# Optimization experiments

Hardware: AMD Instinct MI355X
Metric: run time of the kernel (lower is better)

The kernel has to match this reference:

```python
import jax, jax.numpy as jnp
import numpy as np


def _ln(x, g, b, eps=1e-6):
    m = jnp.mean(x, axis=-1, keepdims=True)
    v = jnp.var(x, axis=-1, keepdims=True)
    return (x - m) * jax.lax.rsqrt(v + eps) * g + b


def setup_inputs():
    key = jax.random.key(0)
    ks = jax.random.split(key, 16)
    B, Hs, Ws, D = 2, 48, 48, 768
    heads, P = 6, 4
    L = Hs * Ws                # feat tokens (single level, 1/16 scale)
    N = 21 * (Hs * Ws // 4)    # query tokens: 16n + 4n + n multi-scale layout
    hidden = int(D * 0.25)
    s = 0.02
    return {
        "query": jax.random.normal(ks[0], (B, N, D), jnp.float32),
        "reference_points": jax.random.uniform(ks[1], (B, N, 1, 2), jnp.float32),
        "feat": jax.random.normal(ks[2], (B, L, D), jnp.float32),
        "spatial_shapes": jnp.array([[Hs, Ws]], jnp.int32),
        "level_start_index": jnp.array([0], jnp.int32),
        "H": Hs, "W": Ws,
        "qn_g": jnp.ones((D,), jnp.float32), "qn_b": jnp.zeros((D,), jnp.float32),
        "fn_g": jnp.ones((D,), jnp.float32), "fn_b": jnp.zeros((D,), jnp.float32),
        "Wv": jax.random.normal(ks[3], (D, D), jnp.float32) * s, "bv": jnp.zeros((D,), jnp.float32),
        "Woff": jax.random.normal(ks[4], (D, heads * P * 2), jnp.float32) * s,
        "boff": jax.random.normal(ks[5], (heads * P * 2,), jnp.float32) * s,
        "Wattn": jax.random.normal(ks[6], (D, heads * P), jnp.float32) * s,
        "battn": jnp.zeros((heads * P,), jnp.float32),
        "Wo": jax.random.normal(ks[7], (D, D), jnp.float32) * s, "bo": jnp.zeros((D,), jnp.float32),
        "ffn_g": jnp.ones((D,), jnp.float32), "ffn_b": jnp.zeros((D,), jnp.float32),
        "W1": jax.random.normal(ks[8], (D, hidden), jnp.float32) * s, "b1": jnp.zeros((hidden,), jnp.float32),
        "dw_w": jax.random.normal(ks[9], (hidden, 1, 3, 3), jnp.float32) * s, "dw_b": jnp.zeros((hidden,), jnp.float32),
        "W2": jax.random.normal(ks[10], (hidden, D), jnp.float32) * s, "b2": jnp.zeros((D,), jnp.float32),
    }


def reference(query, reference_points, feat, spatial_shapes, level_start_index, H, W,
              qn_g, qn_b, fn_g, fn_b, Wv, bv, Woff, boff, Wattn, battn, Wo, bo,
              ffn_g, ffn_b, W1, b1, dw_w, dw_b, W2, b2):
    B, N, D = query.shape
    heads, P = 6, 4
    dh = D // heads
    hidden = W1.shape[1]
    # ---- MSDeformAttn (single level) ----
    qn = _ln(query, qn_g, qn_b)
    fn = _ln(feat, fn_g, fn_b)
    value = (fn @ Wv + bv).reshape(B, -1, heads, dh)           # (B,L,h,dh)
    off = (qn @ Woff + boff).reshape(B, N, heads, 1, P, 2)
    aw = jax.nn.softmax((qn @ Wattn + battn).reshape(B, N, heads, P), axis=-1)
    # offset normalizer = [W_l, H_l]
    norm = jnp.stack([spatial_shapes[..., 1], spatial_shapes[..., 0]], -1).astype(qn.dtype)
    loc = reference_points[:, :, None, :, None, :] + off / norm[None, None, None, :, None, :]
    loc = loc[:, :, :, 0]  # (B,N,heads,P,2) single level
    # grid_sample bilinear, align_corners=False, zero padding
    x = loc[..., 0] * W - 0.5
    y = loc[..., 1] * H - 0.5
    x0 = jnp.floor(x); y0 = jnp.floor(y)
    wx = x - x0; wy = y - y0
    x0 = x0.astype(jnp.int32); y0 = y0.astype(jnp.int32)
    value_t = value.transpose(0, 2, 1, 3)  # (B,heads,L,dh)

    def corner(xi, yi, w):
        valid = (xi >= 0) & (xi < W) & (yi >= 0) & (yi < H)
        idx = jnp.clip(yi, 0, H - 1) * W + jnp.clip(xi, 0, W - 1)
        idx = idx.transpose(0, 2, 1, 3).reshape(B, heads, N * P)
        v = jnp.take_along_axis(value_t, idx[..., None], axis=2)  # (B,h,N*P,dh)
        wm = jnp.where(valid, w, 0.0).transpose(0, 2, 1, 3).reshape(B, heads, N * P)
        return v * wm[..., None]

    sampled = (corner(x0, y0, (1 - wx) * (1 - wy)) + corner(x0 + 1, y0, wx * (1 - wy))
               + corner(x0, y0 + 1, (1 - wx) * wy) + corner(x0 + 1, y0 + 1, wx * wy))
    sampled = sampled.reshape(B, heads, N, P, dh)
    attn = jnp.einsum('bhnpd,bnhp->bnhd', sampled, aw).reshape(B, N, D) @ Wo + bo
    query = query + attn
    # ---- ConvFFN (hidden=dim*cffn_ratio, multi-scale DWConv) ----
    h = _ln(query, ffn_g, ffn_b) @ W1 + b1
    n = N // 21

    def dw(t, hh, ww):
        img = t.transpose(0, 2, 1).reshape(B, hidden, hh, ww)
        out = jax.lax.conv_general_dilated(img, dw_w, (1, 1), 'SAME', feature_group_count=hidden)
        return (out + dw_b[None, :, None, None]).reshape(B, hidden, hh * ww).transpose(0, 2, 1)

    h = jnp.concatenate([dw(h[:, :16 * n], 2 * H, 2 * W),
                         dw(h[:, 16 * n:20 * n], H, W),
                         dw(h[:, 20 * n:], H // 2, W // 2)], axis=1)
    h = jax.nn.gelu(h, approximate=False)
    return query + (h @ W2 + b2)
```

## Files before the change

kernel.cpp:

```cpp
#include <hip/hip_runtime.h>
#include <math.h>

#define BB 2
#define NN 12096
#define LL 2304
#define DD 768
#define HID 192
#define HS 48
#define WS 48

typedef unsigned short u16;
typedef unsigned int u32;
typedef __attribute__((ext_vector_type(8))) __bf16 bf16x8;
typedef __attribute__((ext_vector_type(8))) unsigned short u16x8;
typedef __attribute__((ext_vector_type(4))) float f32x4;

__device__ __forceinline__ u16 f2bf(float f) {
  u32 x = __builtin_bit_cast(u32, f);
  u32 r = (x + 0x7fffu + ((x >> 16) & 1u)) >> 16;
  return (u16)r;
}
__device__ __forceinline__ float bf2f(u16 u) {
  u32 x = ((u32)u) << 16;
  return __builtin_bit_cast(float, x);
}

template <typename T>
__device__ __forceinline__ void ln_row4(const T* xr, const float* g, const float* bta, u16* yr, int t) {
  float v0, v1, v2, v3;
  if constexpr (sizeof(T) == 2) {
    ushort4 u = *(const ushort4*)(xr + 4 * t);
    v0 = bf2f(u.x); v1 = bf2f(u.y); v2 = bf2f(u.z); v3 = bf2f(u.w);
  } else {
    float4 f = *(const float4*)(xr + 4 * t);
    v0 = f.x; v1 = f.y; v2 = f.z; v3 = f.w;
  }
  float s = v0 + v1 + v2 + v3;
  float s2 = v0 * v0 + v1 * v1 + v2 * v2 + v3 * v3;
#pragma unroll
  for (int off = 32; off; off >>= 1) {
    s += __shfl_down(s, off, 64);
    s2 += __shfl_down(s2, off, 64);
  }
  __shared__ float red[6];
  __shared__ float mv[2];
  int wave = t >> 6, lane = t & 63;
  if (lane == 0) { red[wave] = s; red[3 + wave] = s2; }
  __syncthreads();
  if (t == 0) {
    float ts = red[0] + red[1] + red[2];
    float ts2 = red[3] + red[4] + red[5];
    float m = ts * (1.f / DD);
    float var = ts2 * (1.f / DD) - m * m;
    mv[0] = m;
    mv[1] = rsqrtf(var + 1e-6f);
  }
  __syncthreads();
  float m = mv[0], rs = mv[1];
  float4 gv = *(const float4*)(g + 4 * t);
  float4 bv = *(const float4*)(bta + 4 * t);
  ushort4 o;
  o.x = f2bf((v0 - m) * rs * gv.x + bv.x);
  o.y = f2bf((v1 - m) * rs * gv.y + bv.y);
  o.z = f2bf((v2 - m) * rs * gv.z + bv.z);
  o.w = f2bf((v3 - m) * rs * gv.w + bv.w);
  *(ushort4*)(yr + 4 * t) = o;
}

template <typename T>
__global__ __launch_bounds__(192) void ln_kernel(const T* __restrict__ x,
                                                 const float* __restrict__ g,
                                                 const float* __restrict__ bta,
                                                 u16* __restrict__ y) {
  size_t row = blockIdx.x;
  ln_row4<T>(x + row * DD, g, bta, y + row * DD, threadIdx.x);
}

__global__ __launch_bounds__(192) void ln_dual_kernel(const float* __restrict__ xq,
                                                      const float* __restrict__ gq,
                                                      const float* __restrict__ bq,
                                                      u16* __restrict__ yq,
                                                      const float* __restrict__ xf,
                                                      const float* __restrict__ gf,
                                                      const float* __restrict__ bf_,
                                                      u16* __restrict__ yf,
                                                      int Mq) {
  size_t row = blockIdx.x;
  if (row < (size_t)Mq)
    ln_row4<float>(xq + row * DD, gq, bq, yq + row * DD, threadIdx.x);
  else {
    size_t r = row - Mq;
    ln_row4<float>(xf + r * DD, gf, bf_, yf + r * DD, threadIdx.x);
  }
}

template <int BM, int BN, int WM, int WN, int RES, int OUT, int NTSW, int MINW>
__global__ __launch_bounds__(256, MINW) void gemm_bf16(const u16* __restrict__ A,
                                                       const u16* __restrict__ Bt,
                                                       const float* __restrict__ bias,
                                                       const void* __restrict__ res,
                                                       void* __restrict__ Cv,
                                                       int M, int N, int K) {
  constexpr int PM = BM / WM, PN = BN / WN;
  constexpr int FM = PM / 16, FN = PN / 16;
  constexpr int ASEG = BM / 32;
  constexpr int BSEG = BN / 32;
  int bx, by;
  if (NTSW > 0) {
    int flat = blockIdx.x;
    int x = flat & 7, gidx = flat >> 3;
    bx = gidx % NTSW;
    int mg = gidx / NTSW;
    by = mg * 8 + x;
    if (by * BM >= M) return;
  } else {
    bx = blockIdx.x;
    by = blockIdx.y;
  }
  __shared__ u16 As[BM * 64];
  __shared__ u16 Bs[BN * 64];
  int tid = threadIdx.x;
  int w = tid >> 6, lane = tid & 63;
  int rw = w / WN, cw = w % WN;
  int m0 = by * BM, n0 = bx * BN;

  f32x4 acc[FM][FN];
#pragma unroll
  for (int i = 0; i < FM; ++i)
#pragma unroll
    for (int j = 0; j < FN; ++j) acc[i][j] = (f32x4){0.f, 0.f, 0.f, 0.f};

  int lr = lane >> 3;
  int lq = lane & 7;
  int qg = lq ^ lr;
  int l15 = lane & 15, quad = lane >> 4;

  for (int k0 = 0; k0 < K; k0 += 64) {
#pragma unroll
    for (int i = 0; i < ASEG; ++i) {
      int s = w * ASEG + i;
      int row = s * 8 + lr;
      const u16* gp = A + (size_t)(m0 + row) * K + k0 + qg * 8;
      __builtin_amdgcn_global_load_lds(
          (const __attribute__((address_space(1))) void*)gp,
          (__attribute__((address_space(3))) void*)&As[s * 512], 16, 0, 0);
    }
#pragma unroll
    for (int i = 0; i < BSEG; ++i) {
      int s = w * BSEG + i;
      int row = s * 8 + lr;
      const u16* gp = Bt + (size_t)(n0 + row) * K + k0 + qg * 8;
      __builtin_amdgcn_global_load_lds(
          (const __attribute__((address_space(1))) void*)gp,
          (__attribute__((address_space(3))) void*)&Bs[s * 512], 16, 0, 0);
    }
    __syncthreads();
#pragma unroll
    for (int s2 = 0; s2 < 2; ++s2) {
      bf16x8 af[FM], bfr[FN];
#pragma unroll
      for (int mt = 0; mt < FM; ++mt) {
        int rm = rw * PM + mt * 16 + l15;
        int ch = (s2 * 4 + quad) ^ (rm & 7);
        af[mt] = *(const bf16x8*)&As[rm * 64 + ch * 8];
      }
#pragma unroll
      for (int nt = 0; nt < FN; ++nt) {
        int rn = cw * PN + nt * 16 + l15;
        int ch = (s2 * 4 + quad) ^ (rn & 7);
        bfr[nt] = *(const bf16x8*)&Bs[rn * 64 + ch * 8];
      }
#pragma unroll
      for (int mt = 0; mt < FM; ++mt)
#pragma unroll
        for (int nt = 0; nt < FN; ++nt)
          acc[mt][nt] = __builtin_amdgcn_mfma_f32_16x16x32_bf16(af[mt], bfr[nt], acc[mt][nt], 0, 0, 0);
    }
    __syncthreads();
  }

#pragma unroll
  for (int mt = 0; mt < FM; ++mt) {
    int m = m0 + rw * PM + mt * 16 + quad * 4;
#pragma unroll
    for (int nt = 0; nt < FN; ++nt) {
      int n = n0 + cw * PN + nt * 16 + l15;
      float bsv = bias[n];
#pragma unroll
      for (int r = 0; r < 4; ++r) {
        size_t idx = (size_t)(m + r) * N + n;
        float v = acc[mt][nt][r] + bsv;
        if (RES == 1) v += ((const float*)res)[idx];
        if (RES == 2) v += bf2f(((const u16*)res)[idx]);
        if (OUT == 1) ((u16*)Cv)[idx] = f2bf(v);
        else ((float*)Cv)[idx] = v;
      }
    }
  }
}

#define PREP_B0 (DD * DD)
#define PREP_B1 (2 * DD * DD)
#define PREP_B2 (PREP_B1 + HID * DD)
#define PREP_B3 (PREP_B2 + HID * DD)
#define PREP_B4 (PREP_B3 + 128 * DD)
#define PREP_B5 (PREP_B4 + 9 * HID)
__global__ __launch_bounds__(256) void prep_all(const float* __restrict__ Wv, const float* __restrict__ Wo,
                                                const float* __restrict__ W1, const float* __restrict__ W2,
                                                const float* __restrict__ Woff, const float* __restrict__ Wattn,
                                                const float* __restrict__ boff, const float* __restrict__ battn,
                                                const float* __restrict__ dw_w,
                                                u16* __restrict__ Wv_t, u16* __restrict__ Wo_t,
                                                u16* __restrict__ W1_t, u16* __restrict__ W2_t,
                                                u16* __restrict__ Wcat_t, float* __restrict__ bias_cat,
                                                float* __restrict__ dwt) {
  int idx = blockIdx.x * 256 + threadIdx.x;
  if (idx >= PREP_B5) return;
  if (idx < PREP_B0) {
    int n = idx / DD, k = idx - n * DD;
    Wv_t[idx] = f2bf(Wv[(size_t)k * DD + n]);
  } else if (idx < PREP_B1) {
    int l = idx - PREP_B0;
    int n = l / DD, k = l - n * DD;
    Wo_t[l] = f2bf(Wo[(size_t)k * DD + n]);
  } else if (idx < PREP_B2) {
    int l = idx - PREP_B1;
    int n = l / DD, k = l - n * DD;
    W1_t[l] = f2bf(W1[(size_t)k * HID + n]);
  } else if (idx < PREP_B3) {
    int l = idx - PREP_B2;
    int n = l / HID, k = l - n * HID;
    W2_t[l] = f2bf(W2[(size_t)k * DD + n]);
  } else if (idx < PREP_B4) {
    int l = idx - PREP_B3;
    int n = l / DD, k = l - n * DD;
    float v = 0.f;
    if (n < 48) v = Woff[(size_t)k * 48 + n];
    else if (n < 72) v = Wattn[(size_t)k * 24 + (n - 48)];
    Wcat_t[l] = f2bf(v);
    if (l < 128) {
      float b = 0.f;
      if (l < 48) b = boff[l];
      else if (l < 72) b = battn[l - 48];
      bias_cat[l] = b;
    }
  } else {
    int l = idx - PREP_B4;
    int k = l / HID, c = l - k * HID;
    dwt[l] = dw_w[(size_t)c * 9 + k];
  }
}

__global__ __launch_bounds__(192) void sample_kernel(const u16* __restrict__ value,
                                                     const float* __restrict__ off,
                                                     const float* __restrict__ refp,
                                                     u16* __restrict__ s) {
  int flat = blockIdx.x;
  int b = flat & 1;
  int pairi = flat >> 1;
  __shared__ int cidx[192];
  __shared__ float cw[192];
  int t = threadIdx.x;
  if (t < 48) {
    int slr = t / 24;
    int u = t - slr * 24;
    size_t row = (size_t)b * NN + (size_t)pairi * 2 + slr;
    const float* o = off + row * 128;
    int hh = u >> 2, p = u & 3;
    float l0 = o[48 + hh * 4 + 0], l1 = o[48 + hh * 4 + 1];
    float l2 = o[48 + hh * 4 + 2], l3 = o[48 + hh * 4 + 3];
    float mx = fmaxf(fmaxf(l0, l1), fmaxf(l2, l3));
    float e0 = expf(l0 - mx), e1 = expf(l1 - mx), e2 = expf(l2 - mx), e3 = expf(l3 - mx);
    float sum = e0 + e1 + e2 + e3;
    float et = (p == 0) ? e0 : (p == 1) ? e1 : (p == 2) ? e2 : e3;
    float aw = et / sum;
    float x = refp[row * 2 + 0] * (float)WS - 0.5f + o[hh * 8 + p * 2 + 0];
    float y = refp[row * 2 + 1] * (float)HS - 0.5f + o[hh * 8 + p * 2 + 1];
    float xf = floorf(x), yf = floorf(y);
    int x0 = (int)xf, y0 = (int)yf;
    float wx = x - xf, wy = y - yf;
#pragma unroll
    for (int c = 0; c < 4; ++c) {
      int xi = x0 + (c & 1), yi = y0 + (c >> 1);
      float w = ((c & 1) ? wx : 1.f - wx) * ((c >> 1) ? wy : 1.f - wy);
      bool valid = (xi >= 0) && (xi < WS) && (yi >= 0) && (yi < HS);
      int xc = min(max(xi, 0), WS - 1), yc = min(max(yi, 0), HS - 1);
      cidx[slr * 96 + u * 4 + c] = yc * WS + xc;
      cw[slr * 96 + u * 4 + c] = valid ? w * aw : 0.f;
    }
  }
  __syncthreads();
  int glr = t / 96;
  int ci = (t - glr * 96) * 8;
  size_t row = (size_t)b * NN + (size_t)pairi * 2 + glr;
  const u16* vb = value + (size_t)b * LL * DD;
  int h = ci >> 7;
  int base0 = glr * 96 + h * 16;
  u16x8 v[16];
#pragma unroll
  for (int i = 0; i < 16; ++i)
    v[i] = *(const u16x8*)&vb[(size_t)cidx[base0 + i] * DD + ci];
  float a0 = 0.f, a1 = 0.f, a2 = 0.f, a3 = 0.f;
  float a4 = 0.f, a5 = 0.f, a6 = 0.f, a7 = 0.f;
#pragma unroll
  for (int i = 0; i < 16; ++i) {
    float w = cw[base0 + i];
    a0 += w * bf2f(v[i][0]);
    a1 += w * bf2f(v[i][1]);
    a2 += w * bf2f(v[i][2]);
    a3 += w * bf2f(v[i][3]);
    a4 += w * bf2f(v[i][4]);
    a5 += w * bf2f(v[i][5]);
    a6 += w * bf2f(v[i][6]);
    a7 += w * bf2f(v[i][7]);
  }
  u16x8 o8;
  o8[0] = f2bf(a0); o8[1] = f2bf(a1); o8[2] = f2bf(a2); o8[3] = f2bf(a3);
  o8[4] = f2bf(a4); o8[5] = f2bf(a5); o8[6] = f2bf(a6); o8[7] = f2bf(a7);
  *(u16x8*)&s[row * DD + ci] = o8;
}

__global__ __launch_bounds__(256) void dwconv_gelu_kernel(const u16* __restrict__ h,
                                                          const float* __restrict__ wt,
                                                          const float* __restrict__ bias,
                                                          u16* __restrict__ out) {
  size_t idx = (size_t)blockIdx.x * 256 + threadIdx.x;
  if (idx >= (size_t)BB * NN * (HID / 8)) return;
  int c8 = (int)(idx % (HID / 8));
  int c = c8 * 8;
  int rem = (int)(idx / (HID / 8));
  int nidx = rem % NN;
  int b = rem / NN;
  int hh, ww, base;
  if (nidx < 9216)       { hh = 96; ww = 96; base = 0; }
  else if (nidx < 11520) { hh = 48; ww = 48; base = 9216; }
  else                   { hh = 24; ww = 24; base = 11520; }
  int p = nidx - base;
  int y = p / ww, x = p % ww;
  const u16* hb = h + ((size_t)b * NN + base) * HID;

  int nbr[9];
  float msk[9];
#pragma unroll
  for (int dy = -1; dy <= 1; ++dy)
#pragma unroll
    for (int dx = -1; dx <= 1; ++dx) {
      int k = (dy + 1) * 3 + (dx + 1);
      int yy = y + dy, xx = x + dx;
      bool valid = (yy >= 0) && (yy < hh) && (xx >= 0) && (xx < ww);
      int yc = min(max(yy, 0), hh - 1), xc = min(max(xx, 0), ww - 1);
      nbr[k] = yc * ww + xc;
      msk[k] = valid ? 1.f : 0.f;
    }

  u16x8 v[9];
#pragma unroll
  for (int k = 0; k < 9; ++k)
    v[k] = *(const u16x8*)&hb[(size_t)nbr[k] * HID + c];

  float4 b0 = *(const float4*)&bias[c];
  float4 b1 = *(const float4*)&bias[c + 4];
  float a0 = b0.x, a1 = b0.y, a2 = b0.z, a3 = b0.w;
  float a4 = b1.x, a5 = b1.y, a6 = b1.z, a7 = b1.w;
#pragma unroll
  for (int k = 0; k < 9; ++k) {
    float4 w0 = *(const float4*)&wt[k * HID + c];
    float4 w1 = *(const float4*)&wt[k * HID + c + 4];
    float m = msk[k];
    a0 += m * w0.x * bf2f(v[k][0]);
    a1 += m * w0.y * bf2f(v[k][1]);
    a2 += m * w0.z * bf2f(v[k][2]);
    a3 += m * w0.w * bf2f(v[k][3]);
    a4 += m * w1.x * bf2f(v[k][4]);
    a5 += m * w1.y * bf2f(v[k][5]);
    a6 += m * w1.z * bf2f(v[k][6]);
    a7 += m * w1.w * bf2f(v[k][7]);
  }
  const float is2 = 0.70710678118654752f;
  u16x8 o8;
  o8[0] = f2bf(0.5f * a0 * (1.f + erff(a0 * is2)));
  o8[1] = f2bf(0.5f * a1 * (1.f + erff(a1 * is2)));
  o8[2] = f2bf(0.5f * a2 * (1.f + erff(a2 * is2)));
  o8[3] = f2bf(0.5f * a3 * (1.f + erff(a3 * is2)));
  o8[4] = f2bf(0.5f * a4 * (1.f + erff(a4 * is2)));
  o8[5] = f2bf(0.5f * a5 * (1.f + erff(a5 * is2)));
  o8[6] = f2bf(0.5f * a6 * (1.f + erff(a6 * is2)));
  o8[7] = f2bf(0.5f * a7 * (1.f + erff(a7 * is2)));
  *(u16x8*)&out[(size_t)rem * HID + c] = o8;
}

extern "C" void kernel_launch(void* const* d_in, const int* in_sizes, int n_in,
                              void* d_out, int out_size, void* d_ws, size_t ws_size,
                              hipStream_t stream) {
  const float* query = (const float*)d_in[0];
  const float* refp  = (const float*)d_in[1];
  const float* feat  = (const float*)d_in[2];
  const float* qn_g  = (const float*)d_in[7];
  const float* qn_b  = (const float*)d_in[8];
  const float* fn_g  = (const float*)d_in[9];
  const float* fn_b  = (const float*)d_in[10];
  const float* Wv    = (const float*)d_in[11];
  const float* bv    = (const float*)d_in[12];
  const float* Woff  = (const float*)d_in[13];
  const float* boff  = (const float*)d_in[14];
  const float* Wattn = (const float*)d_in[15];
  const float* battn = (const float*)d_in[16];
  const float* Wo    = (const float*)d_in[17];
  const float* bo    = (const float*)d_in[18];
  const float* ffn_g = (const float*)d_in[19];
  const float* ffn_b = (const float*)d_in[20];
  const float* W1    = (const float*)d_in[21];
  const float* b1    = (const float*)d_in[22];
  const float* dw_w  = (const float*)d_in[23];
  const float* dw_b  = (const float*)d_in[24];
  const float* W2    = (const float*)d_in[25];
  const float* b2    = (const float*)d_in[26];
  float* out = (float*)d_out;

  const int Mq = BB * NN;
  const int Mf = BB * LL;

  char* p = (char*)d_ws;
  auto alloc = [&](size_t bytes) { char* r = p; p += (bytes + 255) & ~(size_t)255; return r; };
  u16* qn_bf   = (u16*)alloc((size_t)Mq * DD * 2);
  u16* fn_bf   = (u16*)alloc((size_t)Mf * DD * 2);
  u16* val_bf  = (u16*)alloc((size_t)Mf * DD * 2);
  float* off   = (float*)alloc((size_t)Mq * 128 * 4);
  u16* s_bf    = (u16*)alloc((size_t)Mq * DD * 2);
  u16* q2_bf   = (u16*)alloc((size_t)Mq * DD * 2);
  u16* h_bf    = (u16*)alloc((size_t)Mq * HID * 2);
  u16* h2_bf   = (u16*)alloc((size_t)Mq * HID * 2);
  u16* Wv_t    = (u16*)alloc((size_t)DD * DD * 2);
  u16* Wo_t    = (u16*)alloc((size_t)DD * DD * 2);
  u16* W1_t    = (u16*)alloc((size_t)HID * DD * 2);
  u16* W2_t    = (u16*)alloc((size_t)DD * HID * 2);
  u16* Wcat_t  = (u16*)alloc((size_t)128 * DD * 2);
  float* bias_cat = (float*)alloc(128 * 4);
  float* dwt   = (float*)alloc((size_t)9 * HID * 4);

  prep_all<<<(PREP_B5 + 255) / 256, 256, 0, stream>>>(Wv, Wo, W1, W2, Woff, Wattn, boff, battn, dw_w,
                                                      Wv_t, Wo_t, W1_t, W2_t, Wcat_t, bias_cat, dwt);

  ln_dual_kernel<<<Mq + Mf, 192, 0, stream>>>(query, qn_g, qn_b, qn_bf, feat, fn_g, fn_b, fn_bf, Mq);

  gemm_bf16<128, 64, 2, 2, 0, 1, 12, 4><<<((Mf / 128 + 7) / 8) * 8 * 12, 256, 0, stream>>>(
      fn_bf, Wv_t, bv, nullptr, val_bf, Mf, DD, DD);

  gemm_bf16<64, 64, 2, 2, 0, 0, 2, 4><<<((Mq / 64 + 7) / 8) * 8 * 2, 256, 0, stream>>>(
      qn_bf, Wcat_t, bias_cat, nullptr, off, Mq, 128, DD);

  sample_kernel<<<Mq / 2, 192, 0, stream>>>(val_bf, off, refp, s_bf);

  gemm_bf16<128, 128, 2, 2, 1, 1, 6, 2><<<((Mq / 128 + 7) / 8) * 8 * 6, 256, 0, stream>>>(
      s_bf, Wo_t, bo, query, q2_bf, Mq, DD, DD);

  ln_kernel<u16><<<Mq, 192, 0, stream>>>(q2_bf, ffn_g, ffn_b, qn_bf);

  gemm_bf16<32, 192, 1, 4, 0, 1, 0, 4><<<dim3(1, Mq / 32), 256, 0, stream>>>(
      qn_bf, W1_t, b1, nullptr, h_bf, Mq, HID, DD);

  {
    size_t total = (size_t)BB * NN * (HID / 8);
    int blocks = (int)((total + 255) / 256);
    dwconv_gelu_kernel<<<blocks, 256, 0, stream>>>(h_bf, dwt, dw_b, h2_bf);
  }

  gemm_bf16<128, 128, 2, 2, 2, 0, 6, 2><<<((Mq / 128 + 7) / 8) * 8 * 6, 256, 0, stream>>>(
      h2_bf, W2_t, b2, q2_bf, out, Mq, DD, HID);
}
```

Before: 378.1 us.

## Fuse LayerNorm into offset/attn and FFN-W1 GEMMs, shrink offset width to 96

```diff
diff --git a/kernel.cpp b/kernel.cpp
--- a/kernel.cpp
+++ b/kernel.cpp
@@ -74,24 +74,6 @@
                                                  u16* __restrict__ y) {
   size_t row = blockIdx.x;
   ln_row4<T>(x + row * DD, g, bta, y + row * DD, threadIdx.x);
-}
-
-__global__ __launch_bounds__(192) void ln_dual_kernel(const float* __restrict__ xq,
-                                                      const float* __restrict__ gq,
-                                                      const float* __restrict__ bq,
-                                                      u16* __restrict__ yq,
-                                                      const float* __restrict__ xf,
-                                                      const float* __restrict__ gf,
-                                                      const float* __restrict__ bf_,
-                                                      u16* __restrict__ yf,
-                                                      int Mq) {
-  size_t row = blockIdx.x;
-  if (row < (size_t)Mq)
-    ln_row4<float>(xq + row * DD, gq, bq, yq + row * DD, threadIdx.x);
-  else {
-    size_t r = row - Mq;
-    ln_row4<float>(xf + r * DD, gf, bf_, yf + r * DD, threadIdx.x);
-  }
 }
 
 template <int BM, int BN, int WM, int WN, int RES, int OUT, int NTSW, int MINW>
@@ -199,11 +181,141 @@
   }
 }
 
+template <typename T, int BN, int OUT>
+__global__ __launch_bounds__(256, 2) void gemm_ln(const T* __restrict__ A,
+                                                  const float* __restrict__ g,
+                                                  const float* __restrict__ bta,
+                                                  const u16* __restrict__ Bt,
+                                                  const float* __restrict__ bias,
+                                                  void* __restrict__ Cv,
+                                                  int N) {
+  constexpr int BM = 32;
+  constexpr int PN = BN / 2;
+  constexpr int FN = PN / 16;
+  constexpr int BSEG = BN / 32;
+  __shared__ u16 As[12 * BM * 64];
+  __shared__ u16 Bs[BN * 64];
+  int tid = threadIdx.x;
+  int w = tid >> 6, lane = tid & 63;
+  int rw = w >> 1, cw = w & 1;
+  int m0 = blockIdx.y * BM, n0 = blockIdx.x * BN;
+
+  int r = tid >> 3;
+  int q = tid & 7;
+  const T* arow = A + (size_t)(m0 + r) * DD;
+  float s = 0.f, s2 = 0.f;
+#pragma unroll
+  for (int i = 0; i < 12; ++i) {
+    int slot = q + i * 8;
+    int j = slot >> 3, pp = slot & 7;
+    int k = j * 64 + (pp ^ (r & 7)) * 8;
+    if constexpr (sizeof(T) == 2) {
+      u16x8 v = *(const u16x8*)(arow + k);
+#pragma unroll
+      for (int e = 0; e < 8; ++e) { float f = bf2f(v[e]); s += f; s2 += f * f; }
+    } else {
+      float4 f0 = *(const float4*)(arow + k);
+      float4 f1 = *(const float4*)(arow + k + 4);
+      s += f0.x + f0.y + f0.z + f0.w + f1.x + f1.y + f1.z + f1.w;
+      s2 += f0.x*f0.x + f0.y*f0.y + f0.z*f0.z + f0.w*f0.w
+          + f1.x*f1.x + f1.y*f1.y + f1.z*f1.z + f1.w*f1.w;
+    }
+  }
+#pragma unroll
+  for (int msk = 1; msk < 8; msk <<= 1) {
+    s += __shfl_xor(s, msk, 64);
+    s2 += __shfl_xor(s2, msk, 64);
+  }
+  float mean = s * (1.f / DD);
+  float rs = rsqrtf(s2 * (1.f / DD) - mean * mean + 1e-6f);
+
+#pragma unroll
+  for (int i = 0; i < 12; ++i) {
+    int slot = q + i * 8;
+    int j = slot >> 3, pp = slot & 7;
+    int k = j * 64 + (pp ^ (r & 7)) * 8;
+    float x[8];
+    if constexpr (sizeof(T) == 2) {
+      u16x8 v = *(const u16x8*)(arow + k);
+#pragma unroll
+      for (int e = 0; e < 8; ++e) x[e] = bf2f(v[e]);
+    } else {
+      float4 f0 = *(const float4*)(arow + k);
+      float4 f1 = *(const float4*)(arow + k + 4);
+      x[0]=f0.x; x[1]=f0.y; x[2]=f0.z; x[3]=f0.w;
+      x[4]=f1.x; x[5]=f1.y; x[6]=f1.z; x[7]=f1.w;
+    }
+    float4 g0 = *(const float4*)(g + k);
+    float4 g1 = *(const float4*)(g + k + 4);
+    float4 b0 = *(const float4*)(bta + k);
+    float4 b1 = *(const float4*)(bta + k + 4);
+    float gg[8] = {g0.x,g0.y,g0.z,g0.w,g1.x,g1.y,g1.z,g1.w};
+    float bb[8] = {b0.x,b0.y,b0.z,b0.w,b1.x,b1.y,b1.z,b1.w};
+    u16x8 o;
+#pragma unroll
+    for (int e = 0; e < 8; ++e) o[e] = f2bf((x[e] - mean) * rs * gg[e] + bb[e]);
+    *(u16x8*)&As[((size_t)j * BM + r) * 64 + pp * 8] = o;
+  }
+  __syncthreads();
+
+  f32x4 acc[FN];
+#pragma unroll
+  for (int j = 0; j < FN; ++j) acc[j] = (f32x4){0.f, 0.f, 0.f, 0.f};
+  int lr = lane >> 3;
+  int lq = lane & 7;
+  int qg = lq ^ lr;
+  int l15 = lane & 15, quad = lane >> 4;
+
+  for (int j = 0; j < 12; ++j) {
+#pragma unroll
+    for (int i = 0; i < BSEG; ++i) {
+      int sg = w * BSEG + i;
+      int row = sg * 8 + lr;
+      const u16* gp = Bt + (size_t)(n0 + row) * DD + j * 64 + qg * 8;
+      __builtin_amdgcn_global_load_lds(
+          (const __attribute__((address_space(1))) void*)gp,
+          (__attribute__((address_space(3))) void*)&Bs[sg * 512], 16, 0, 0);
+    }
+    __syncthreads();
+#pragma unroll
+    for (int s2i = 0; s2i < 2; ++s2i) {
+      int rm = rw * 16 + l15;
+      int ch = (s2i * 4 + quad) ^ (rm & 7);
+      bf16x8 af = *(const bf16x8*)&As[((size_t)j * BM + rm) * 64 + ch * 8];
+      bf16x8 bfr[FN];
+#pragma unroll
+      for (int nt = 0; nt < FN; ++nt) {
+        int rn = cw * PN + nt * 16 + l15;
+        int chb = (s2i * 4 + quad) ^ (rn & 7);
+        bfr[nt] = *(const bf16x8*)&Bs[rn * 64 + chb * 8];
+      }
+#pragma unroll
+      for (int nt = 0; nt < FN; ++nt)
+        acc[nt] = __builtin_amdgcn_mfma_f32_16x16x32_bf16(af, bfr[nt], acc[nt], 0, 0, 0);
+    }
+    __syncthreads();
+  }
+
+  int m = m0 + rw * 16 + quad * 4;
+#pragma unroll
+  for (int nt = 0; nt < FN; ++nt) {
+    int n = n0 + cw * PN + nt * 16 + l15;
+    float bsv = bias[n];
+#pragma unroll
+    for (int r4 = 0; r4 < 4; ++r4) {
+      size_t idx = (size_t)(m + r4) * N + n;
+      float v = acc[nt][r4] + bsv;
+      if (OUT == 1) ((u16*)Cv)[idx] = f2bf(v);
+      else ((float*)Cv)[idx] = v;
+    }
+  }
+}
+
 #define PREP_B0 (DD * DD)
 #define PREP_B1 (2 * DD * DD)
 #define PREP_B2 (PREP_B1 + HID * DD)
 #define PREP_B3 (PREP_B2 + HID * DD)
-#define PREP_B4 (PREP_B3 + 128 * DD)
+#define PREP_B4 (PREP_B3 + 96 * DD)
 #define PREP_B5 (PREP_B4 + 9 * HID)
 __global__ __launch_bounds__(256) void prep_all(const float* __restrict__ Wv, const float* __restrict__ Wo,
                                                 const float* __restrict__ W1, const float* __restrict__ W2,
@@ -238,7 +350,7 @@
     if (n < 48) v = Woff[(size_t)k * 48 + n];
     else if (n < 72) v = Wattn[(size_t)k * 24 + (n - 48)];
     Wcat_t[l] = f2bf(v);
-    if (l < 128) {
+    if (l < 96) {
       float b = 0.f;
       if (l < 48) b = boff[l];
       else if (l < 72) b = battn[l - 48];
@@ -265,7 +377,7 @@
     int slr = t / 24;
     int u = t - slr * 24;
     size_t row = (size_t)b * NN + (size_t)pairi * 2 + slr;
-    const float* o = off + row * 128;
+    const float* o = off + row * 96;
     int hh = u >> 2, p = u & 3;
     float l0 = o[48 + hh * 4 + 0], l1 = o[48 + hh * 4 + 1];
     float l2 = o[48 + hh * 4 + 2], l3 = o[48 + hh * 4 + 3];
@@ -422,10 +534,9 @@
 
   char* p = (char*)d_ws;
   auto alloc = [&](size_t bytes) { char* r = p; p += (bytes + 255) & ~(size_t)255; return r; };
-  u16* qn_bf   = (u16*)alloc((size_t)Mq * DD * 2);
   u16* fn_bf   = (u16*)alloc((size_t)Mf * DD * 2);
   u16* val_bf  = (u16*)alloc((size_t)Mf * DD * 2);
-  float* off   = (float*)alloc((size_t)Mq * 128 * 4);
+  float* off   = (float*)alloc((size_t)Mq * 96 * 4);
   u16* s_bf    = (u16*)alloc((size_t)Mq * DD * 2);
   u16* q2_bf   = (u16*)alloc((size_t)Mq * DD * 2);
   u16* h_bf    = (u16*)alloc((size_t)Mq * HID * 2);
@@ -434,30 +545,28 @@
   u16* Wo_t    = (u16*)alloc((size_t)DD * DD * 2);
   u16* W1_t    = (u16*)alloc((size_t)HID * DD * 2);
   u16* W2_t    = (u16*)alloc((size_t)DD * HID * 2);
-  u16* Wcat_t  = (u16*)alloc((size_t)128 * DD * 2);
-  float* bias_cat = (float*)alloc(128 * 4);
+  u16* Wcat_t  = (u16*)alloc((size_t)96 * DD * 2);
+  float* bias_cat = (float*)alloc(96 * 4);
   float* dwt   = (float*)alloc((size_t)9 * HID * 4);
 
   prep_all<<<(PREP_B5 + 255) / 256, 256, 0, stream>>>(Wv, Wo, W1, W2, Woff, Wattn, boff, battn, dw_w,
                                                       Wv_t, Wo_t, W1_t, W2_t, Wcat_t, bias_cat, dwt);
 
-  ln_dual_kernel<<<Mq + Mf, 192, 0, stream>>>(query, qn_g, qn_b, qn_bf, feat, fn_g, fn_b, fn_bf, Mq);
+  ln_kernel<float><<<Mf, 192, 0, stream>>>(feat, fn_g, fn_b, fn_bf);
 
   gemm_bf16<128, 64, 2, 2, 0, 1, 12, 4><<<((Mf / 128 + 7) / 8) * 8 * 12, 256, 0, stream>>>(
       fn_bf, Wv_t, bv, nullptr, val_bf, Mf, DD, DD);
 
-  gemm_bf16<64, 64, 2, 2, 0, 0, 2, 4><<<((Mq / 64 + 7) / 8) * 8 * 2, 256, 0, stream>>>(
-      qn_bf, Wcat_t, bias_cat, nullptr, off, Mq, 128, DD);
+  gemm_ln<float, 96, 0><<<dim3(1, Mq / 32), 256, 0, stream>>>(
+      query, qn_g, qn_b, Wcat_t, bias_cat, off, 96);
 
   sample_kernel<<<Mq / 2, 192, 0, stream>>>(val_bf, off, refp, s_bf);
 
   gemm_bf16<128, 128, 2, 2, 1, 1, 6, 2><<<((Mq / 128 + 7) / 8) * 8 * 6, 256, 0, stream>>>(
       s_bf, Wo_t, bo, query, q2_bf, Mq, DD, DD);
 
-  ln_kernel<u16><<<Mq, 192, 0, stream>>>(q2_bf, ffn_g, ffn_b, qn_bf);
-
-  gemm_bf16<32, 192, 1, 4, 0, 1, 0, 4><<<dim3(1, Mq / 32), 256, 0, stream>>>(
-      qn_bf, W1_t, b1, nullptr, h_bf, Mq, HID, DD);
+  gemm_ln<u16, 96, 1><<<dim3(2, Mq / 32), 256, 0, stream>>>(
+      q2_bf, ffn_g, ffn_b, W1_t, b1, h_bf, HID);
 
   {
     size_t total = (size_t)BB * NN * (HID / 8);
```

Result: no change. 377.2 us (-0.2%).
